# Optimization experiments

Hardware: AMD Instinct MI355X
Metric: run time of the kernel (lower is better)

The kernel has to match this reference:

```python
import jax, jax.numpy as jnp
import numpy as np

EPS = 1e-5
NUM_HEADS = 8

def layernorm(x, g, b):
    m = x.mean(-1, keepdims=True)
    v = ((x - m) ** 2).mean(-1, keepdims=True)
    return (x - m) / jnp.sqrt(v + EPS) * g + b

def mha(x, qkv_w, qkv_b, proj_w, proj_b):
    # x: [B, N, C]; weights stored [in, out] (transposed torch Linear)
    B, N, C = x.shape
    hd = C // NUM_HEADS
    scale = hd ** -0.5
    qkv = (x @ qkv_w + qkv_b).reshape(B, N, 3, NUM_HEADS, hd)
    qkv = jnp.transpose(qkv, (2, 0, 3, 1, 4))  # [3, B, H, N, hd]
    q, k, v = qkv[0], qkv[1], qkv[2]
    attn = jax.nn.softmax(jnp.einsum('bhnd,bhmd->bhnm', q, k) * scale, axis=-1)
    o = jnp.einsum('bhnm,bhmd->bhnd', attn, v)
    o = jnp.transpose(o, (0, 2, 1, 3)).reshape(B, N, C)
    return o @ proj_w + proj_b

def gelu(x):
    return jax.nn.gelu(x, approximate=False)

def setup_inputs() -> dict:
    key = jax.random.key(0)
    C, H = 512, 2048
    B, P, NI = 2, 196, 16
    N = 1 + NI * P
    ks = jax.random.split(key, 16)
    s = 0.02
    d = {
        'x': jax.random.normal(ks[0], (B, N, C), jnp.float32),
        'num_patches_per_image': P,
        'ln1_g': jnp.ones((C,)), 'ln1_b': jnp.zeros((C,)),
        'ln2_g': jnp.ones((C,)), 'ln2_b': jnp.zeros((C,)),
        'ln3_g': jnp.ones((C,)), 'ln3_b': jnp.zeros((C,)),
        'g_qkv_w': jax.random.normal(ks[1], (C, 3 * C)) * s,
        'g_qkv_b': jnp.zeros((3 * C,)),
        'g_proj_w': jax.random.normal(ks[2], (C, C)) * s,
        'g_proj_b': jnp.zeros((C,)),
        'l_qkv_w': jax.random.normal(ks[3], (C, 3 * C)) * s,
        'l_qkv_b': jnp.zeros((3 * C,)),
        'l_proj_w': jax.random.normal(ks[4], (C, C)) * s,
        'l_proj_b': jnp.zeros((C,)),
        'mlp_w1': jax.random.normal(ks[5], (C, H)) * s,
        'mlp_b1': jnp.zeros((H,)),
        'mlp_w2': jax.random.normal(ks[6], (H, C)) * s,
        'mlp_b2': jnp.zeros((C,)),
    }
    return d

def reference(x, num_patches_per_image, ln1_g, ln1_b, ln2_g, ln2_b, ln3_g, ln3_b,
              g_qkv_w, g_qkv_b, g_proj_w, g_proj_b,
              l_qkv_w, l_qkv_b, l_proj_w, l_proj_b,
              mlp_w1, mlp_b1, mlp_w2, mlp_b2):
    B, N, C = x.shape
    P = int(num_patches_per_image)
    NI = (N - 1) // P
    # global attention over all tokens (incl. CLS)
    x = x + mha(layernorm(x, ln1_g, ln1_b), g_qkv_w, g_qkv_b, g_proj_w, g_proj_b)
    cls_tok = x[:, 0:1, :]
    patches = x[:, 1:, :]
    # local attention: block-diagonal per-image mask == independent attention
    # within each image block (masked entries underflow to exactly 0 in softmax)
    pn = layernorm(patches, ln2_g, ln2_b).reshape(B * NI, P, C)
    local = mha(pn, l_qkv_w, l_qkv_b, l_proj_w, l_proj_b).reshape(B, NI * P, C)
    patches = patches + local
    x = jnp.concatenate([cls_tok, patches], axis=1)
    h = layernorm(x, ln3_g, ln3_b)
    h = gelu(h @ mlp_w1 + mlp_b1) @ mlp_w2 + mlp_b2
    return x + h
```

## Files before the change

kernel.cpp:

```cpp
#include <hip/hip_runtime.h>
#include <math.h>

typedef __attribute__((ext_vector_type(8))) short bf16x8;
typedef __attribute__((ext_vector_type(4))) short bf16x4_t;
typedef __attribute__((ext_vector_type(4))) float f32x4;
typedef __attribute__((ext_vector_type(4))) unsigned int u32x4;

typedef const __attribute__((address_space(1))) unsigned int glb_u32;
typedef __attribute__((address_space(3))) unsigned int lds_u32;
#define GLOAD_LDS16(g, l) __builtin_amdgcn_global_load_lds( \
    (glb_u32*)(const void*)(g), (lds_u32*)(void*)(l), 16, 0, 0)

static __device__ __forceinline__ float4 ld4(const float* p) {
    return *reinterpret_cast<const float4*>(p);
}
static __device__ __forceinline__ unsigned short f2bf(float f) {
    unsigned int u = __float_as_uint(f);
    u += 0x7fffu + ((u >> 16) & 1u);
    return (unsigned short)(u >> 16);
}

__global__ __launch_bounds__(64) void ln_kernel(
    const float* __restrict__ in, const float* __restrict__ g,
    const float* __restrict__ bta, unsigned short* __restrict__ out, int mode)
{
    int r = blockIdx.x;
    int lane = threadIdx.x;
    int in_r = mode ? (r + 1 + r / 3136) : r;
    const float* xp = in + (size_t)in_r * 512 + lane * 8;
    float4 v0 = ld4(xp), v1 = ld4(xp + 4);
    float s  = v0.x + v0.y + v0.z + v0.w + v1.x + v1.y + v1.z + v1.w;
    float sq = v0.x*v0.x + v0.y*v0.y + v0.z*v0.z + v0.w*v0.w
             + v1.x*v1.x + v1.y*v1.y + v1.z*v1.z + v1.w*v1.w;
    #pragma unroll
    for (int off = 32; off; off >>= 1) {
        s  += __shfl_xor(s, off);
        sq += __shfl_xor(sq, off);
    }
    float mean = s * (1.f / 512.f);
    float var  = fmaxf(sq * (1.f / 512.f) - mean * mean, 0.f);
    float rstd = rsqrtf(var + 1e-5f);
    float4 g0 = ld4(g + lane * 8),   g1 = ld4(g + lane * 8 + 4);
    float4 b0 = ld4(bta + lane * 8), b1 = ld4(bta + lane * 8 + 4);
    float o0 = (v0.x - mean) * rstd * g0.x + b0.x;
    float o1 = (v0.y - mean) * rstd * g0.y + b0.y;
    float o2 = (v0.z - mean) * rstd * g0.z + b0.z;
    float o3 = (v0.w - mean) * rstd * g0.w + b0.w;
    float o4 = (v1.x - mean) * rstd * g1.x + b1.x;
    float o5 = (v1.y - mean) * rstd * g1.y + b1.y;
    float o6 = (v1.z - mean) * rstd * g1.z + b1.z;
    float o7 = (v1.w - mean) * rstd * g1.w + b1.w;
    u32x4 pk;
    pk[0] = (unsigned int)f2bf(o0) | ((unsigned int)f2bf(o1) << 16);
    pk[1] = (unsigned int)f2bf(o2) | ((unsigned int)f2bf(o3) << 16);
    pk[2] = (unsigned int)f2bf(o4) | ((unsigned int)f2bf(o5) << 16);
    pk[3] = (unsigned int)f2bf(o6) | ((unsigned int)f2bf(o7) << 16);
    *(u32x4*)(out + (size_t)r * 512 + lane * 8) = pk;
}

struct TransArgs {
    const float* src[6];
    unsigned short* dst[6];
    int N[6], K[6], off[6];
};

__global__ __launch_bounds__(256) void transpose_all(TransArgs a)
{
    __shared__ unsigned short tile[32][34];
    int t = blockIdx.x;
    int i = 0;
    #pragma unroll
    for (int j = 1; j < 6; ++j) if (t >= a.off[j]) i = j;
    int rel = t - a.off[i];
    int tx_n = a.N[i] >> 5;
    int bx = (rel % tx_n) * 32, by = (rel / tx_n) * 32;
    const float* W = a.src[i];
    unsigned short* WT = a.dst[i];
    int K = a.K[i], N = a.N[i];
    int tx = threadIdx.x & 31, ty = threadIdx.x >> 5;
    #pragma unroll
    for (int r = 0; r < 32; r += 8)
        tile[ty + r][tx] = f2bf(W[(size_t)(by + ty + r) * N + bx + tx]);
    __syncthreads();
    #pragma unroll
    for (int r = 0; r < 32; r += 8)
        WT[(size_t)(bx + ty + r) * K + by + tx] = tile[tx][ty + r];
}

template<int BM, int BN, int OUT_BF16>
__global__ __launch_bounds__(256) void mfma_gemm(
    const unsigned short* __restrict__ A, const unsigned short* __restrict__ WT,
    const float* __restrict__ bias, const float* __restrict__ resid,
    void* __restrict__ outp, int M, int N, int K,
    int rowmap, int act,
    unsigned short* __restrict__ vt_out,
    int vtNs, unsigned int vtMagic, int vtNsP, int vtColBase)
{
    constexpr int FI = BM / 32, FJ = BN / 32;
    constexpr int AL = BM / 64, BL = BN / 64;
    __shared__ __align__(16) unsigned short As[2][BM * 32];
    __shared__ __align__(16) unsigned short Bs[2][BN * 32];

    int tid = threadIdx.x;
    int m0 = blockIdx.x * BM, n0 = blockIdx.y * BN;
    int w = tid >> 6, l = tid & 63;
    int wm = (w >> 1) * (BM / 2), wn = (w & 1) * (BN / 2);
    int lr = l & 15, lg = l >> 4;

    int lrow = l >> 2;
    int lcol = (l & 3) * 8;

    f32x4 zero = {0.f, 0.f, 0.f, 0.f};
    f32x4 acc[FI][FJ];
    #pragma unroll
    for (int i = 0; i < FI; ++i)
        #pragma unroll
        for (int j = 0; j < FJ; ++j) acc[i][j] = zero;

#define STAGE(buf, kk) do { \
    _Pragma("unroll") \
    for (int q = 0; q < AL; ++q) { \
        int rb = (w * AL + q) * 16; \
        GLOAD_LDS16(A + (size_t)(m0 + rb + lrow) * K + (kk) + lcol, \
                    &As[buf][rb * 32]); \
    } \
    _Pragma("unroll") \
    for (int q = 0; q < BL; ++q) { \
        int rb = (w * BL + q) * 16; \
        GLOAD_LDS16(WT + (size_t)(n0 + rb + lrow) * K + (kk) + lcol, \
                    &Bs[buf][rb * 32]); \
    } \
} while (0)

    int nk = K >> 5;
    STAGE(0, 0);
    STAGE(1, 32);
    for (int s = 0; s < nk; ++s) {
        int cur = s & 1;
        if (s + 1 < nk) {
            if constexpr (AL + BL == 2)
                asm volatile("s_waitcnt vmcnt(2)" ::: "memory");
            else if constexpr (AL + BL == 3)
                asm volatile("s_waitcnt vmcnt(3)" ::: "memory");
            else
                asm volatile("s_waitcnt vmcnt(4)" ::: "memory");
        } else {
            asm volatile("s_waitcnt vmcnt(0)" ::: "memory");
        }
        __builtin_amdgcn_s_barrier();

        bf16x8 af[FI], bfr[FJ];
        #pragma unroll
        for (int i = 0; i < FI; ++i)
            af[i] = *(const bf16x8*)&As[cur][(wm + i * 16 + lr) * 32 + lg * 8];
        #pragma unroll
        for (int j = 0; j < FJ; ++j)
            bfr[j] = *(const bf16x8*)&Bs[cur][(wn + j * 16 + lr) * 32 + lg * 8];
        asm volatile("s_waitcnt lgkmcnt(0)" ::: "memory");
        __builtin_amdgcn_sched_barrier(0);
        __builtin_amdgcn_s_barrier();
        if (s + 2 < nk) STAGE(cur, (s + 2) * 32);

        #pragma unroll
        for (int i = 0; i < FI; ++i)
            #pragma unroll
            for (int j = 0; j < FJ; ++j)
                acc[i][j] = __builtin_amdgcn_mfma_f32_16x16x32_bf16(
                    af[i], bfr[j], acc[i][j], 0, 0, 0);
    }
#undef STAGE

    int rowW = vt_out ? vtColBase : N;
    #pragma unroll
    for (int i = 0; i < FI; ++i) {
        #pragma unroll
        for (int r = 0; r < 4; ++r) {
            int row = m0 + wm + i * 16 + lg * 4 + r;
            if (row >= M) continue;
            int orow = rowmap ? (row + 1 + row / 3136) : row;
            #pragma unroll
            for (int j = 0; j < FJ; ++j) {
                int col = n0 + wn + j * 16 + lr;
                if (col >= N) continue;
                float v = acc[i][j][r] + bias[col];
                if (act) v = 0.5f * v * (1.f + erff(v * 0.70710678118654752f));
                if (resid) v += resid[(size_t)orow * N + col];
                if (vt_out && col >= vtColBase) {
                    unsigned int bb = (unsigned int)(((unsigned long long)(unsigned int)row * vtMagic) >> 32);
                    int nn = row - (int)bb * vtNs;
                    vt_out[((size_t)bb * 512 + (col - vtColBase)) * vtNsP + nn] = f2bf(v);
                } else if (OUT_BF16) {
                    ((unsigned short*)outp)[(size_t)orow * rowW + col] = f2bf(v);
                } else {
                    ((float*)outp)[(size_t)orow * rowW + col] = v;
                }
            }
        }
    }
}

__global__ __launch_bounds__(256) void attn_mfma(
    const unsigned short* __restrict__ qk, const unsigned short* __restrict__ vT,
    unsigned short* __restrict__ o, int Ns, int NsP)
{
    __shared__ __align__(16) unsigned short Ks[2][64 * 64];
    __shared__ __align__(16) unsigned short Vs[2][64 * 64];

    int tid = threadIdx.x;
    int h = blockIdx.y, b = blockIdx.z;
    int mb = b * Ns;
    int l = tid & 63, w = tid >> 6;
    int g = l >> 4, c16 = l & 15;

    int qrow = blockIdx.x * 64 + w * 16 + c16;
    int qr = (qrow < Ns ? qrow : Ns - 1) + mb;
    const unsigned short* qp = qk + (size_t)qr * 1024 + h * 64;
    bf16x8 bQ0 = *(const bf16x8*)(qp + g * 8);
    bf16x8 bQ1 = *(const bf16x8*)(qp + 32 + g * 8);

    f32x4 zero = {0.f, 0.f, 0.f, 0.f};
    f32x4 Oacc[4] = {zero, zero, zero, zero};
    float mrun = -1e30f, lrun = 0.f;

    int r0 = tid >> 3, ch = tid & 7;
    int r1 = r0 + 32;
    int kd0 = r0 * 64 + ((ch ^ ((r0 & 7) ^ (r0 >> 3))) * 8);
    int kd1 = r1 * 64 + ((ch ^ ((r1 & 7) ^ (r1 >> 3))) * 8);
    const unsigned short* kbase = qk + (size_t)mb * 1024 + 512 + h * 64 + ch * 8;
    const unsigned short* vb0 = vT + ((size_t)b * 512 + h * 64 + r0) * NsP + ch * 8;
    const unsigned short* vb1 = vT + ((size_t)b * 512 + h * 64 + r1) * NsP + ch * 8;

    int ka[4][2];
    #pragma unroll
    for (int f = 0; f < 4; ++f) {
        int key = 16 * f + c16;
        int swz = (key & 7) ^ (key >> 3);
        ka[f][0] = key * 64 + ((g ^ swz) * 8);
        ka[f][1] = key * 64 + (((4 + g) ^ swz) * 8);
    }
    int va[4][4];
    #pragma unroll
    for (int j = 0; j < 4; ++j) {
        int d = 16 * j + c16;
        int sd = (d & 7) ^ (d >> 3);
        #pragma unroll
        for (int t = 0; t < 4; ++t) {
            int hc = 4 * t + g;
            va[j][t] = d * 64 + (((hc >> 1) ^ sd) * 8) + ((g & 1) * 4);
        }
    }

    const float SCL = 0.125f * 1.4426950408889634f;
    int nt = (Ns + 63) >> 6;
    int tail = Ns & 63;

    u32x4 kv0, kv1, vv0, vv1;
#define LOADT(kt) do { \
    int kr0 = (kt) * 64 + r0; if (kr0 >= Ns) kr0 = Ns - 1; \
    int kr1 = (kt) * 64 + r1; if (kr1 >= Ns) kr1 = Ns - 1; \
    kv0 = *(const u32x4*)(kbase + (size_t)kr0 * 1024); \
    kv1 = *(const u32x4*)(kbase + (size_t)kr1 * 1024); \
    vv0 = *(const u32x4*)(vb0 + (kt) * 64); \
    vv1 = *(const u32x4*)(vb1 + (kt) * 64); \
} while (0)
#define STORET(buf) do { \
    *(u32x4*)&Ks[buf][kd0] = kv0; \
    *(u32x4*)&Ks[buf][kd1] = kv1; \
    *(u32x4*)&Vs[buf][kd0] = vv0; \
    *(u32x4*)&Vs[buf][kd1] = vv1; \
} while (0)

    LOADT(0);
    STORET(0);
    if (nt > 1) LOADT(1);
    __syncthreads();

    int cur = 0;
    for (int kt = 0; kt < nt; ++kt) {
        if (kt + 1 < nt) {
            STORET(cur ^ 1);
            if (kt + 2 < nt) LOADT(kt + 2);
        }
        const unsigned short* Kc = &Ks[cur][0];
        const unsigned short* Vc = &Vs[cur][0];

        f32x4 st[4];
        #pragma unroll
        for (int f = 0; f < 4; ++f) {
            bf16x8 a0 = *(const bf16x8*)&Kc[ka[f][0]];
            bf16x8 a1 = *(const bf16x8*)&Kc[ka[f][1]];
            f32x4 a = zero;
            a = __builtin_amdgcn_mfma_f32_16x16x32_bf16(a0, bQ0, a, 0, 0, 0);
            a = __builtin_amdgcn_mfma_f32_16x16x32_bf16(a1, bQ1, a, 0, 0, 0);
            st[f] = a;
        }

        float sv[16];
        #pragma unroll
        for (int f = 0; f < 4; ++f)
            #pragma unroll
            for (int r = 0; r < 4; ++r) sv[4 * f + r] = st[f][r];
        if (kt == nt - 1 && tail) {
            #pragma unroll
            for (int f = 0; f < 4; ++f)
                #pragma unroll
                for (int r = 0; r < 4; ++r)
                    if (16 * f + 4 * g + r >= tail) sv[4 * f + r] = -1e30f;
        }
        float m01 = fmaxf(sv[0], sv[1]), m23 = fmaxf(sv[2], sv[3]);
        float m45 = fmaxf(sv[4], sv[5]), m67 = fmaxf(sv[6], sv[7]);
        float m89 = fmaxf(sv[8], sv[9]), mab = fmaxf(sv[10], sv[11]);
        float mcd = fmaxf(sv[12], sv[13]), mef = fmaxf(sv[14], sv[15]);
        float mloc = fmaxf(fmaxf(fmaxf(m01, m23), fmaxf(m45, m67)),
                           fmaxf(fmaxf(m89, mab), fmaxf(mcd, mef)));
        if (!__all(mloc - mrun <= 64.f)) {
            mloc = fmaxf(mloc, __shfl_xor(mloc, 16));
            mloc = fmaxf(mloc, __shfl_xor(mloc, 32));
            float mnew = fmaxf(mrun, mloc);
            float sc = exp2f((mrun - mnew) * SCL);
            lrun *= sc;
            #pragma unroll
            for (int j = 0; j < 4; ++j) {
                Oacc[j][0] *= sc; Oacc[j][1] *= sc;
                Oacc[j][2] *= sc; Oacc[j][3] *= sc;
            }
            mrun = mnew;
        }
        float nl = mrun * SCL;
        #pragma unroll
        for (int e = 0; e < 16; ++e) {
            sv[e] = exp2f(fmaf(sv[e], SCL, -nl));
            lrun += sv[e];
        }

        union { unsigned int u[4]; bf16x8 v; } plo, phi;
        #pragma unroll
        for (int wi = 0; wi < 4; ++wi) {
            asm("v_cvt_pk_bf16_f32 %0, %1, %2"
                : "=v"(plo.u[wi]) : "v"(sv[2 * wi]), "v"(sv[2 * wi + 1]));
            asm("v_cvt_pk_bf16_f32 %0, %1, %2"
                : "=v"(phi.u[wi]) : "v"(sv[8 + 2 * wi]), "v"(sv[8 + 2 * wi + 1]));
        }

        #pragma unroll
        for (int j = 0; j < 4; ++j) {
            bf16x4_t t0 = *(const bf16x4_t*)&Vc[va[j][0]];
            bf16x4_t t1 = *(const bf16x4_t*)&Vc[va[j][1]];
            bf16x4_t t2 = *(const bf16x4_t*)&Vc[va[j][2]];
            bf16x4_t t3 = *(const bf16x4_t*)&Vc[va[j][3]];
            bf16x8 aVlo = __builtin_shufflevector(t0, t1, 0, 1, 2, 3, 4, 5, 6, 7);
            bf16x8 aVhi = __builtin_shufflevector(t2, t3, 0, 1, 2, 3, 4, 5, 6, 7);
            Oacc[j] = __builtin_amdgcn_mfma_f32_16x16x32_bf16(aVlo, plo.v, Oacc[j], 0, 0, 0);
            Oacc[j] = __builtin_amdgcn_mfma_f32_16x16x32_bf16(aVhi, phi.v, Oacc[j], 0, 0, 0);
        }

        __syncthreads();
        cur ^= 1;
    }
#undef LOADT
#undef STORET

    lrun += __shfl_xor(lrun, 16);
    lrun += __shfl_xor(lrun, 32);

    if (qrow < Ns) {
        float inv = 1.f / lrun;
        unsigned short* op = o + (size_t)(mb + qrow) * 512 + h * 64;
        #pragma unroll
        for (int j = 0; j < 4; ++j) {
            unsigned int u0, u1;
            asm("v_cvt_pk_bf16_f32 %0, %1, %2"
                : "=v"(u0) : "v"(Oacc[j][0] * inv), "v"(Oacc[j][1] * inv));
            asm("v_cvt_pk_bf16_f32 %0, %1, %2"
                : "=v"(u1) : "v"(Oacc[j][2] * inv), "v"(Oacc[j][3] * inv));
            uint2 stv; stv.x = u0; stv.y = u1;
            *(uint2*)(op + 16 * j + 4 * g) = stv;
        }
    }
}

extern "C" void kernel_launch(void* const* d_in, const int* in_sizes, int n_in,
                              void* d_out, int out_size, void* d_ws, size_t ws_size,
                              hipStream_t stream)
{
    const float* x       = (const float*)d_in[0];
    const float* ln1_g   = (const float*)d_in[2];
    const float* ln1_b   = (const float*)d_in[3];
    const float* ln2_g   = (const float*)d_in[4];
    const float* ln2_b   = (const float*)d_in[5];
    const float* ln3_g   = (const float*)d_in[6];
    const float* ln3_b   = (const float*)d_in[7];
    const float* g_qkv_w = (const float*)d_in[8];
    const float* g_qkv_b = (const float*)d_in[9];
    const float* g_proj_w= (const float*)d_in[10];
    const float* g_proj_b= (const float*)d_in[11];
    const float* l_qkv_w = (const float*)d_in[12];
    const float* l_qkv_b = (const float*)d_in[13];
    const float* l_proj_w= (const float*)d_in[14];
    const float* l_proj_b= (const float*)d_in[15];
    const float* mlp_w1  = (const float*)d_in[16];
    const float* mlp_b1  = (const float*)d_in[17];
    const float* mlp_w2  = (const float*)d_in[18];
    const float* mlp_b2  = (const float*)d_in[19];

    float* out = (float*)d_out;

    unsigned short* buf_a = (unsigned short*)d_ws;
    unsigned short* buf_b = buf_a + (size_t)6274 * 512;
    unsigned short* vTb   = buf_b + (size_t)6274 * 2048;
    unsigned short* wbf   = vTb + (size_t)3276800 + 64;
    unsigned short* g_qkv_t  = wbf;
    unsigned short* g_proj_t = g_qkv_t + 1536 * 512;
    unsigned short* l_qkv_t  = g_proj_t + 512 * 512;
    unsigned short* l_proj_t = l_qkv_t + 1536 * 512;
    unsigned short* w1_t     = l_proj_t + 512 * 512;
    unsigned short* w2_t     = w1_t + (size_t)2048 * 512;

    unsigned int M3137 = (unsigned int)((0x100000000ULL + 3136) / 3137);
    unsigned int M196  = (unsigned int)((0x100000000ULL + 195) / 196);

    TransArgs ta;
    ta.src[0] = g_qkv_w;  ta.dst[0] = g_qkv_t;  ta.N[0] = 1536; ta.K[0] = 512;  ta.off[0] = 0;
    ta.src[1] = g_proj_w; ta.dst[1] = g_proj_t; ta.N[1] = 512;  ta.K[1] = 512;  ta.off[1] = 768;
    ta.src[2] = l_qkv_w;  ta.dst[2] = l_qkv_t;  ta.N[2] = 1536; ta.K[2] = 512;  ta.off[2] = 1024;
    ta.src[3] = l_proj_w; ta.dst[3] = l_proj_t; ta.N[3] = 512;  ta.K[3] = 512;  ta.off[3] = 1792;
    ta.src[4] = mlp_w1;   ta.dst[4] = w1_t;     ta.N[4] = 2048; ta.K[4] = 512;  ta.off[4] = 2048;
    ta.src[5] = mlp_w2;   ta.dst[5] = w2_t;     ta.N[5] = 512;  ta.K[5] = 2048; ta.off[5] = 3072;
    transpose_all<<<4096, 256, 0, stream>>>(ta);

    ln_kernel<<<6274, 64, 0, stream>>>(x, ln1_g, ln1_b, buf_a, 0);
    mfma_gemm<128,128,1><<<dim3(50, 12), 256, 0, stream>>>(
        buf_a, g_qkv_t, g_qkv_b, nullptr, buf_b, 6274, 1536, 512, 0, 0,
        vTb, 3137, M3137, 3144, 1024);
    attn_mfma<<<dim3(50, 8, 2), 256, 0, stream>>>(buf_b, vTb, buf_a, 3137, 3144);
    mfma_gemm<64,64,0><<<dim3(99, 8), 256, 0, stream>>>(
        buf_a, g_proj_t, g_proj_b, x, out, 6274, 512, 512, 0, 0,
        nullptr, 0, 0u, 0, 0);
    ln_kernel<<<6272, 64, 0, stream>>>(out, ln2_g, ln2_b, buf_a, 1);
    mfma_gemm<128,128,1><<<dim3(49, 12), 256, 0, stream>>>(
        buf_a, l_qkv_t, l_qkv_b, nullptr, buf_b, 6272, 1536, 512, 0, 0,
        vTb, 196, M196, 200, 1024);
    attn_mfma<<<dim3(4, 8, 32), 256, 0, stream>>>(buf_b, vTb, buf_a, 196, 200);
    mfma_gemm<64,64,0><<<dim3(98, 8), 256, 0, stream>>>(
        buf_a, l_proj_t, l_proj_b, out, out, 6272, 512, 512, 1, 0,
        nullptr, 0, 0u, 0, 0);
    ln_kernel<<<6274, 64, 0, stream>>>(out, ln3_g, ln3_b, buf_a, 0);
    mfma_gemm<128,128,1><<<dim3(50, 16), 256, 0, stream>>>(
        buf_a, w1_t, mlp_b1, nullptr, buf_b, 6274, 2048, 512, 0, 1,
        nullptr, 0, 0u, 0, 0);
    mfma_gemm<64,64,0><<<dim3(99, 8), 256, 0, stream>>>(
        buf_b, w2_t, mlp_b2, out, out, 6274, 512, 2048, 0, 0,
        nullptr, 0, 0u, 0, 0);
}
```

Measured before the change: 381.4 us.

## Split attention key loop across two wave groups with LDS softmax merge

The attention kernel now runs 8 waves per block, where two groups of four waves each handle alternate 64-key halves of every 128-key tile for the same 64 queries. At the end the partial outputs, maxima and sums are merged through LDS before the output is written. This doubles the waves working on each query block, so the sequential key loop is half as long and more latency can be hidden. In exchange, the double-buffered prefetch pipeline is replaced by a single buffer with two barriers per tile, and a merge step is added.

```diff
diff --git a/kernel.cpp b/kernel.cpp
--- a/kernel.cpp
+++ b/kernel.cpp
@@ -199,20 +199,20 @@
     }
 }
 
-__global__ __launch_bounds__(256) void attn_mfma(
+__global__ __launch_bounds__(512) void attn_mfma8(
     const unsigned short* __restrict__ qk, const unsigned short* __restrict__ vT,
     unsigned short* __restrict__ o, int Ns, int NsP)
 {
-    __shared__ __align__(16) unsigned short Ks[2][64 * 64];
-    __shared__ __align__(16) unsigned short Vs[2][64 * 64];
+    __shared__ __align__(16) unsigned short lds[4 * 4096];
 
     int tid = threadIdx.x;
     int h = blockIdx.y, b = blockIdx.z;
     int mb = b * Ns;
     int l = tid & 63, w = tid >> 6;
+    int qg = w & 3, kp = w >> 2;
     int g = l >> 4, c16 = l & 15;
 
-    int qrow = blockIdx.x * 64 + w * 16 + c16;
+    int qrow = blockIdx.x * 64 + qg * 16 + c16;
     int qr = (qrow < Ns ? qrow : Ns - 1) + mb;
     const unsigned short* qp = qk + (size_t)qr * 1024 + h * 64;
     bf16x8 bQ0 = *(const bf16x8*)(qp + g * 8);
@@ -223,12 +223,12 @@
     float mrun = -1e30f, lrun = 0.f;
 
     int r0 = tid >> 3, ch = tid & 7;
-    int r1 = r0 + 32;
-    int kd0 = r0 * 64 + ((ch ^ ((r0 & 7) ^ (r0 >> 3))) * 8);
-    int kd1 = r1 * 64 + ((ch ^ ((r1 & 7) ^ (r1 >> 3))) * 8);
+    int kd = r0 * 64 + ((ch ^ ((r0 & 7) ^ (r0 >> 3))) * 8);
     const unsigned short* kbase = qk + (size_t)mb * 1024 + 512 + h * 64 + ch * 8;
-    const unsigned short* vb0 = vT + ((size_t)b * 512 + h * 64 + r0) * NsP + ch * 8;
-    const unsigned short* vb1 = vT + ((size_t)b * 512 + h * 64 + r1) * NsP + ch * 8;
+    const unsigned short* vbase = vT + ((size_t)b * 512 + h * 64 + r0) * NsP + ch * 8;
+
+    unsigned short* Kp = lds + kp * 4096;
+    unsigned short* Vp = lds + 8192 + kp * 4096;
 
     int ka[4][2];
     #pragma unroll
@@ -251,44 +251,36 @@
     }
 
     const float SCL = 0.125f * 1.4426950408889634f;
-    int nt = (Ns + 63) >> 6;
-    int tail = Ns & 63;
+    int nt = (Ns + 127) >> 7;
 
     u32x4 kv0, kv1, vv0, vv1;
 #define LOADT(kt) do { \
-    int kr0 = (kt) * 64 + r0; if (kr0 >= Ns) kr0 = Ns - 1; \
-    int kr1 = (kt) * 64 + r1; if (kr1 >= Ns) kr1 = Ns - 1; \
+    int kr0 = (kt) * 128 + r0;      if (kr0 >= Ns) kr0 = Ns - 1; \
+    int kr1 = (kt) * 128 + 64 + r0; if (kr1 >= Ns) kr1 = Ns - 1; \
     kv0 = *(const u32x4*)(kbase + (size_t)kr0 * 1024); \
     kv1 = *(const u32x4*)(kbase + (size_t)kr1 * 1024); \
-    vv0 = *(const u32x4*)(vb0 + (kt) * 64); \
-    vv1 = *(const u32x4*)(vb1 + (kt) * 64); \
+    vv0 = *(const u32x4*)(vbase + (kt) * 128); \
+    vv1 = *(const u32x4*)(vbase + (kt) * 128 + 64); \
 } while (0)
-#define STORET(buf) do { \
-    *(u32x4*)&Ks[buf][kd0] = kv0; \
-    *(u32x4*)&Ks[buf][kd1] = kv1; \
-    *(u32x4*)&Vs[buf][kd0] = vv0; \
-    *(u32x4*)&Vs[buf][kd1] = vv1; \
+#define STORET() do { \
+    *(u32x4*)&lds[kd] = kv0; \
+    *(u32x4*)&lds[4096 + kd] = kv1; \
+    *(u32x4*)&lds[8192 + kd] = vv0; \
+    *(u32x4*)&lds[12288 + kd] = vv1; \
 } while (0)
 
     LOADT(0);
-    STORET(0);
-    if (nt > 1) LOADT(1);
-    __syncthreads();
-
-    int cur = 0;
     for (int kt = 0; kt < nt; ++kt) {
-        if (kt + 1 < nt) {
-            STORET(cur ^ 1);
-            if (kt + 2 < nt) LOADT(kt + 2);
-        }
-        const unsigned short* Kc = &Ks[cur][0];
-        const unsigned short* Vc = &Vs[cur][0];
+        __syncthreads();
+        STORET();
+        __syncthreads();
+        if (kt + 1 < nt) LOADT(kt + 1);
 
         f32x4 st[4];
         #pragma unroll
         for (int f = 0; f < 4; ++f) {
-            bf16x8 a0 = *(const bf16x8*)&Kc[ka[f][0]];
-            bf16x8 a1 = *(const bf16x8*)&Kc[ka[f][1]];
+            bf16x8 a0 = *(const bf16x8*)&Kp[ka[f][0]];
+            bf16x8 a1 = *(const bf16x8*)&Kp[ka[f][1]];
             f32x4 a = zero;
             a = __builtin_amdgcn_mfma_f32_16x16x32_bf16(a0, bQ0, a, 0, 0, 0);
             a = __builtin_amdgcn_mfma_f32_16x16x32_bf16(a1, bQ1, a, 0, 0, 0);
@@ -300,12 +292,13 @@
         for (int f = 0; f < 4; ++f)
             #pragma unroll
             for (int r = 0; r < 4; ++r) sv[4 * f + r] = st[f][r];
-        if (kt == nt - 1 && tail) {
+        int valid = Ns - kt * 128 - kp * 64;
+        if (valid < 64) {
             #pragma unroll
             for (int f = 0; f < 4; ++f)
                 #pragma unroll
                 for (int r = 0; r < 4; ++r)
-                    if (16 * f + 4 * g + r >= tail) sv[4 * f + r] = -1e30f;
+                    if (16 * f + 4 * g + r >= valid) sv[4 * f + r] = -1e30f;
         }
         float m01 = fmaxf(sv[0], sv[1]), m23 = fmaxf(sv[2], sv[3]);
         float m45 = fmaxf(sv[4], sv[5]), m67 = fmaxf(sv[6], sv[7]);
@@ -344,37 +337,59 @@
 
         #pragma unroll
         for (int j = 0; j < 4; ++j) {
-            bf16x4_t t0 = *(const bf16x4_t*)&Vc[va[j][0]];
-            bf16x4_t t1 = *(const bf16x4_t*)&Vc[va[j][1]];
-            bf16x4_t t2 = *(const bf16x4_t*)&Vc[va[j][2]];
-            bf16x4_t t3 = *(const bf16x4_t*)&Vc[va[j][3]];
+            bf16x4_t t0 = *(const bf16x4_t*)&Vp[va[j][0]];
+            bf16x4_t t1 = *(const bf16x4_t*)&Vp[va[j][1]];
+            bf16x4_t t2 = *(const bf16x4_t*)&Vp[va[j][2]];
+            bf16x4_t t3 = *(const bf16x4_t*)&Vp[va[j][3]];
             bf16x8 aVlo = __builtin_shufflevector(t0, t1, 0, 1, 2, 3, 4, 5, 6, 7);
             bf16x8 aVhi = __builtin_shufflevector(t2, t3, 0, 1, 2, 3, 4, 5, 6, 7);
             Oacc[j] = __builtin_amdgcn_mfma_f32_16x16x32_bf16(aVlo, plo.v, Oacc[j], 0, 0, 0);
             Oacc[j] = __builtin_amdgcn_mfma_f32_16x16x32_bf16(aVhi, phi.v, Oacc[j], 0, 0, 0);
         }
-
-        __syncthreads();
-        cur ^= 1;
     }
 #undef LOADT
 #undef STORET
 
-    lrun += __shfl_xor(lrun, 16);
-    lrun += __shfl_xor(lrun, 32);
-
-    if (qrow < Ns) {
-        float inv = 1.f / lrun;
-        unsigned short* op = o + (size_t)(mb + qrow) * 512 + h * 64;
+    __syncthreads();
+    float* xch = (float*)&lds[0];
+    float* slot = xch + (size_t)(qg * 64 + l) * 20;
+    if (kp == 1) {
+        #pragma unroll
+        for (int j = 0; j < 4; ++j)
+            *(f32x4*)(slot + 4 * j) = Oacc[j];
+        slot[16] = mrun;
+        slot[17] = lrun;
+    }
+    __syncthreads();
+    if (kp == 0) {
+        float m1 = slot[16], l1 = slot[17];
+        float mm = fmaxf(mrun, m1);
+        float s0 = exp2f((mrun - mm) * SCL);
+        float s1 = exp2f((m1 - mm) * SCL);
+        lrun = lrun * s0 + l1 * s1;
         #pragma unroll
         for (int j = 0; j < 4; ++j) {
-            unsigned int u0, u1;
-            asm("v_cvt_pk_bf16_f32 %0, %1, %2"
-                : "=v"(u0) : "v"(Oacc[j][0] * inv), "v"(Oacc[j][1] * inv));
-            asm("v_cvt_pk_bf16_f32 %0, %1, %2"
-                : "=v"(u1) : "v"(Oacc[j][2] * inv), "v"(Oacc[j][3] * inv));
-            uint2 stv; stv.x = u0; stv.y = u1;
-            *(uint2*)(op + 16 * j + 4 * g) = stv;
+            f32x4 o1 = *(const f32x4*)(slot + 4 * j);
+            Oacc[j][0] = Oacc[j][0] * s0 + o1[0] * s1;
+            Oacc[j][1] = Oacc[j][1] * s0 + o1[1] * s1;
+            Oacc[j][2] = Oacc[j][2] * s0 + o1[2] * s1;
+            Oacc[j][3] = Oacc[j][3] * s0 + o1[3] * s1;
+        }
+        lrun += __shfl_xor(lrun, 16);
+        lrun += __shfl_xor(lrun, 32);
+        if (qrow < Ns) {
+            float inv = 1.f / lrun;
+            unsigned short* op = o + (size_t)(mb + qrow) * 512 + h * 64;
+            #pragma unroll
+            for (int j = 0; j < 4; ++j) {
+                unsigned int u0, u1;
+                asm("v_cvt_pk_bf16_f32 %0, %1, %2"
+                    : "=v"(u0) : "v"(Oacc[j][0] * inv), "v"(Oacc[j][1] * inv));
+                asm("v_cvt_pk_bf16_f32 %0, %1, %2"
+                    : "=v"(u1) : "v"(Oacc[j][2] * inv), "v"(Oacc[j][3] * inv));
+                uint2 stv; stv.x = u0; stv.y = u1;
+                *(uint2*)(op + 16 * j + 4 * g) = stv;
+            }
         }
     }
 }
@@ -432,7 +447,7 @@
     mfma_gemm<128,128,1><<<dim3(50, 12), 256, 0, stream>>>(
         buf_a, g_qkv_t, g_qkv_b, nullptr, buf_b, 6274, 1536, 512, 0, 0,
         vTb, 3137, M3137, 3144, 1024);
-    attn_mfma<<<dim3(50, 8, 2), 256, 0, stream>>>(buf_b, vTb, buf_a, 3137, 3144);
+    attn_mfma8<<<dim3(50, 8, 2), 512, 0, stream>>>(buf_b, vTb, buf_a, 3137, 3144);
     mfma_gemm<64,64,0><<<dim3(99, 8), 256, 0, stream>>>(
         buf_a, g_proj_t, g_proj_b, x, out, 6274, 512, 512, 0, 0,
         nullptr, 0, 0u, 0, 0);
@@ -440,7 +455,7 @@
     mfma_gemm<128,128,1><<<dim3(49, 12), 256, 0, stream>>>(
         buf_a, l_qkv_t, l_qkv_b, nullptr, buf_b, 6272, 1536, 512, 0, 0,
         vTb, 196, M196, 200, 1024);
-    attn_mfma<<<dim3(4, 8, 32), 256, 0, stream>>>(buf_b, vTb, buf_a, 196, 200);
+    attn_mfma8<<<dim3(4, 8, 32), 512, 0, stream>>>(buf_b, vTb, buf_a, 196, 200);
     mfma_gemm<64,64,0><<<dim3(98, 8), 256, 0, stream>>>(
         buf_a, l_proj_t, l_proj_b, out, out, 6272, 512, 512, 1, 0,
         nullptr, 0, 0u, 0, 0);
```

Result: faster. 363.9 us (-4.6%).
